# Performance work log

Measured on AMD Instinct MI355X. Metric: run time of the kernel, lower is better.

The kernel has to match this reference:

```python
import jax, jax.numpy as jnp
import numpy as np

N, E, IN_DIM, HID, HEADS, LAYERS = 50000, 320000, 128, 128, 4, 2
C = HID // HEADS  # per-head channels = 32
EPS = 1e-5


def _init(key, shape, fan_in):
    return jax.random.normal(key, shape, dtype=jnp.float32) / np.sqrt(fan_in)


def setup_inputs() -> dict:
    key = jax.random.key(0)
    ks = jax.random.split(key, 20)
    x = jax.random.normal(ks[0], (N, IN_DIM), dtype=jnp.float32)
    edge_index = jax.random.randint(ks[1], (2, E), 0, N, dtype=jnp.int64)
    edge_attr = jax.random.uniform(ks[2], (E, 1), dtype=jnp.float32)
    inp = {
        "x": x, "edge_index": edge_index, "edge_attr": edge_attr,
        "W_in": _init(ks[3], (IN_DIM, HID), IN_DIM),
        "b_in": jnp.zeros((HID,), jnp.float32),
        # per-layer TransformerConv params, stacked on leading layer axis
        "Wq": _init(ks[4], (LAYERS, HID, HID), HID),
        "bq": jnp.zeros((LAYERS, HID), jnp.float32),
        "Wk": _init(ks[5], (LAYERS, HID, HID), HID),
        "bk": jnp.zeros((LAYERS, HID), jnp.float32),
        "Wv": _init(ks[6], (LAYERS, HID, HID), HID),
        "bv": jnp.zeros((LAYERS, HID), jnp.float32),
        "We": _init(ks[7], (LAYERS, 1, HID), 1),          # lin_edge, bias=False
        "Wskip": _init(ks[8], (LAYERS, HID, HID), HID),   # root/skip projection
        "bskip": jnp.zeros((LAYERS, HID), jnp.float32),
        "Wbeta": _init(ks[9], (LAYERS, 3 * HID, 1), 3 * HID),  # lin_beta, bias=False
        "bn_gamma": jnp.ones((LAYERS, HID), jnp.float32),
        "bn_beta": jnp.zeros((LAYERS, HID), jnp.float32),
    }
    return inp


def _transformer_conv(h, src, tgt, edge_attr, Wq, bq, Wk, bk, Wv, bv, We, Wskip, bskip, Wbeta):
    n = h.shape[0]
    q = (h @ Wq + bq).reshape(n, HEADS, C)
    k = (h @ Wk + bk).reshape(n, HEADS, C)
    v = (h @ Wv + bv).reshape(n, HEADS, C)
    e = (edge_attr @ We).reshape(-1, HEADS, C)          # [E,H,C] edge embedding
    k_j = k[src] + e                                     # gather source keys
    alpha = jnp.einsum('ehc,ehc->eh', q[tgt], k_j) / jnp.sqrt(jnp.float32(C))
    amax = jax.ops.segment_max(alpha, tgt, num_segments=n)   # softmax over in-edges per target
    ex = jnp.exp(alpha - amax[tgt])
    denom = jax.ops.segment_sum(ex, tgt, num_segments=n)
    a = ex / denom[tgt]                                  # [E,H]
    msg = (v[src] + e) * a[..., None]
    out = jax.ops.segment_sum(msg, tgt, num_segments=n).reshape(n, HID)
    x_r = h @ Wskip + bskip                              # root weight
    beta = jax.nn.sigmoid(jnp.concatenate([out, x_r, out - x_r], axis=-1) @ Wbeta)
    return beta * x_r + (1.0 - beta) * out


def _batchnorm(h, gamma, beta):
    mu = h.mean(axis=0)
    var = h.var(axis=0)
    return gamma * (h - mu) * jax.lax.rsqrt(var + EPS) + beta


def reference(x, edge_index, edge_attr, W_in, b_in, Wq, bq, Wk, bk, Wv, bv, We, Wskip, bskip, Wbeta, bn_gamma, bn_beta):
    src, tgt = edge_index[0], edge_index[1]
    h = jax.nn.relu(x @ W_in + b_in)
    for l in range(LAYERS):
        h_res = h
        h = _transformer_conv(h, src, tgt, edge_attr, Wq[l], bq[l], Wk[l], bk[l], Wv[l], bv[l], We[l], Wskip[l], bskip[l], Wbeta[l])
        h = jax.nn.relu(_batchnorm(h, bn_gamma[l], bn_beta[l]))
        h = h + h_res
    return h
```

## Files before the change

kernel.cpp:

```cpp
#include <hip/hip_runtime.h>
#include <hip/hip_bf16.h>
#include <math.h>

#define EPS 1e-5f

typedef __attribute__((ext_vector_type(8))) short bf16x8;
typedef __attribute__((ext_vector_type(4))) float f32x4;

__device__ __forceinline__ unsigned short f2bf(float f) {
    unsigned u = __float_as_uint(f);
    unsigned r = (u + 0x7FFFu + ((u >> 16) & 1u)) >> 16;
    return (unsigned short)r;
}
__device__ __forceinline__ unsigned f2bf2(float lo, float hi) {
    return (unsigned)f2bf(lo) | ((unsigned)f2bf(hi) << 16);
}
__device__ __forceinline__ float bf2f(unsigned short u) {
    return __uint_as_float((unsigned)u << 16);
}
__device__ __forceinline__ void bfu2(unsigned u, float& lo, float& hi) {
    lo = __uint_as_float(u << 16);
    hi = __uint_as_float(u & 0xFFFF0000u);
}

__global__ __launch_bounds__(256) void prep(const float* __restrict__ x,
                                            unsigned short* __restrict__ xbf, int n4,
                                            const float* __restrict__ W0, const float* __restrict__ W1,
                                            const float* __restrict__ W2, const float* __restrict__ W3,
                                            const float* __restrict__ W4, const float* __restrict__ W5,
                                            const float* __restrict__ W6, const float* __restrict__ W7,
                                            const float* __restrict__ W8, unsigned short* __restrict__ Bpack,
                                            int* __restrict__ deg, int N,
                                            int nConv, int nPack) {
    int b = blockIdx.x;
    if (b < nConv) {
        int i = b * 256 + threadIdx.x;
        if (i < n4) {
            float4 v = ((const float4*)x)[i];
            ushort4 o = make_ushort4(f2bf(v.x), f2bf(v.y), f2bf(v.z), f2bf(v.w));
            ((ushort4*)xbf)[i] = o;
        }
    } else if (b < nConv + nPack) {
        int t = (b - nConv) * 256 + threadIdx.x;
        if (t < 9 * 16384) {
            int mat = t >> 14, r = t & 16383;
            const float* W;
            switch (mat) {
                case 0: W = W0; break; case 1: W = W1; break; case 2: W = W2; break;
                case 3: W = W3; break; case 4: W = W4; break; case 5: W = W5; break;
                case 6: W = W6; break; case 7: W = W7; break; default: W = W8; break;
            }
            int j = r & 7, lane = (r >> 3) & 63, nt = (r >> 9) & 7, kc = r >> 12;
            int k = kc * 32 + (lane >> 4) * 8 + j;
            int n = (lane & 15) * 8 + nt;
            Bpack[t] = f2bf(W[k * 128 + n]);
        }
    } else {
        int i = (b - nConv - nPack) * 256 + threadIdx.x;
        if (i < N) deg[i] = 0;
    }
}

template <int ACT, int WBF>
__global__ __launch_bounds__(256) void gemm_mfma(const unsigned short* __restrict__ Abf,
                                                 const unsigned short* __restrict__ Bp,
                                                 const float* __restrict__ bias,
                                                 float* __restrict__ C,
                                                 unsigned short* __restrict__ Cbf, int M) {
    int wave = threadIdx.x >> 6, lane = threadIdx.x & 63;
    int base = blockIdx.x * 64 + wave * 16;
    int m = lane & 15, kg = lane >> 4;
    int arow = base + m; if (arow >= M) arow = M - 1;
    const unsigned short* Aptr = Abf + (size_t)arow * 128 + kg * 8;
    f32x4 acc[8];
#pragma unroll
    for (int nt = 0; nt < 8; ++nt) acc[nt] = (f32x4)(0.f);
#pragma unroll
    for (int kc = 0; kc < 4; ++kc) {
        bf16x8 a = *(const bf16x8*)(Aptr + kc * 32);
        const unsigned short* bp = Bp + (size_t)kc * 4096 + (size_t)lane * 8;
#pragma unroll
        for (int nt = 0; nt < 8; ++nt) {
            bf16x8 b = *(const bf16x8*)(bp + nt * 512);
            acc[nt] = __builtin_amdgcn_mfma_f32_16x16x32_bf16(a, b, acc[nt], 0, 0, 0);
        }
    }
    int col0 = lane & 15;
    int r0 = base + (lane >> 4) * 4;
    float4 bl = *(const float4*)&bias[col0 * 8];
    float4 bh = *(const float4*)&bias[col0 * 8 + 4];
#pragma unroll
    for (int r = 0; r < 4; ++r) {
        int ro = r0 + r;
        if (ro < M) {
            float v0 = acc[0][r] + bl.x, v1 = acc[1][r] + bl.y;
            float v2 = acc[2][r] + bl.z, v3 = acc[3][r] + bl.w;
            float v4 = acc[4][r] + bh.x, v5 = acc[5][r] + bh.y;
            float v6 = acc[6][r] + bh.z, v7 = acc[7][r] + bh.w;
            if (ACT) {
                v0 = fmaxf(v0, 0.f); v1 = fmaxf(v1, 0.f); v2 = fmaxf(v2, 0.f); v3 = fmaxf(v3, 0.f);
                v4 = fmaxf(v4, 0.f); v5 = fmaxf(v5, 0.f); v6 = fmaxf(v6, 0.f); v7 = fmaxf(v7, 0.f);
            }
            size_t o = (size_t)ro * 128 + col0 * 8;
            *(float4*)&C[o]     = make_float4(v0, v1, v2, v3);
            *(float4*)&C[o + 4] = make_float4(v4, v5, v6, v7);
            if (WBF)
                *(uint4*)&Cbf[o] = make_uint4(f2bf2(v0, v1), f2bf2(v2, v3),
                                              f2bf2(v4, v5), f2bf2(v6, v7));
        }
    }
}

__global__ __launch_bounds__(256) void gemm_qk(const unsigned short* __restrict__ Abf,
                                               const unsigned short* __restrict__ Bq,
                                               const unsigned short* __restrict__ Bk,
                                               const float* __restrict__ bq,
                                               const float* __restrict__ bk,
                                               unsigned short* __restrict__ qbf,
                                               unsigned short* __restrict__ kvbf, int M) {
    int wave = threadIdx.x >> 6, lane = threadIdx.x & 63;
    int base = blockIdx.x * 64 + wave * 16;
    int m = lane & 15, kg = lane >> 4;
    int arow = base + m; if (arow >= M) arow = M - 1;
    const unsigned short* Aptr = Abf + (size_t)arow * 128 + kg * 8;
    f32x4 aq[8], ak[8];
#pragma unroll
    for (int nt = 0; nt < 8; ++nt) { aq[nt] = (f32x4)(0.f); ak[nt] = (f32x4)(0.f); }
#pragma unroll
    for (int kc = 0; kc < 4; ++kc) {
        bf16x8 a = *(const bf16x8*)(Aptr + kc * 32);
        size_t boff = (size_t)kc * 4096 + (size_t)lane * 8;
#pragma unroll
        for (int nt = 0; nt < 8; ++nt) {
            bf16x8 b0 = *(const bf16x8*)(Bq + boff + nt * 512);
            aq[nt] = __builtin_amdgcn_mfma_f32_16x16x32_bf16(a, b0, aq[nt], 0, 0, 0);
            bf16x8 b1 = *(const bf16x8*)(Bk + boff + nt * 512);
            ak[nt] = __builtin_amdgcn_mfma_f32_16x16x32_bf16(a, b1, ak[nt], 0, 0, 0);
        }
    }
    int col0 = lane & 15;
    int r0 = base + (lane >> 4) * 4;
    float4 bql = *(const float4*)&bq[col0 * 8], bqh = *(const float4*)&bq[col0 * 8 + 4];
    float4 bkl = *(const float4*)&bk[col0 * 8], bkh = *(const float4*)&bk[col0 * 8 + 4];
#pragma unroll
    for (int r = 0; r < 4; ++r) {
        int ro = r0 + r;
        if (ro < M) {
            size_t qo = (size_t)ro * 128 + col0 * 8;
            size_t kvo = (size_t)ro * 256 + col0 * 8;
            *(uint4*)&qbf[qo] = make_uint4(
                f2bf2(aq[0][r] + bql.x, aq[1][r] + bql.y), f2bf2(aq[2][r] + bql.z, aq[3][r] + bql.w),
                f2bf2(aq[4][r] + bqh.x, aq[5][r] + bqh.y), f2bf2(aq[6][r] + bqh.z, aq[7][r] + bqh.w));
            *(uint4*)&kvbf[kvo] = make_uint4(
                f2bf2(ak[0][r] + bkl.x, ak[1][r] + bkl.y), f2bf2(ak[2][r] + bkl.z, ak[3][r] + bkl.w),
                f2bf2(ak[4][r] + bkh.x, ak[5][r] + bkh.y), f2bf2(ak[6][r] + bkh.z, ak[7][r] + bkh.w));
        }
    }
}

__global__ __launch_bounds__(256) void gemm_vs(const unsigned short* __restrict__ Abf,
                                               const unsigned short* __restrict__ Bv,
                                               const unsigned short* __restrict__ Bs,
                                               const float* __restrict__ bv,
                                               const float* __restrict__ bs,
                                               unsigned short* __restrict__ kvbf,
                                               unsigned short* __restrict__ xrbf,
                                               float* __restrict__ bstatZ, int M) {
    if (blockIdx.x == 0) {
        ((float2*)bstatZ)[threadIdx.x] = make_float2(0.f, 0.f);
        ((float2*)bstatZ)[256 + threadIdx.x] = make_float2(0.f, 0.f);
        ((float2*)bstatZ)[512 + threadIdx.x] = make_float2(0.f, 0.f);
        ((float2*)bstatZ)[768 + threadIdx.x] = make_float2(0.f, 0.f);
    }
    int wave = threadIdx.x >> 6, lane = threadIdx.x & 63;
    int base = blockIdx.x * 64 + wave * 16;
    int m = lane & 15, kg = lane >> 4;
    int arow = base + m; if (arow >= M) arow = M - 1;
    const unsigned short* Aptr = Abf + (size_t)arow * 128 + kg * 8;
    f32x4 av[8], as_[8];
#pragma unroll
    for (int nt = 0; nt < 8; ++nt) { av[nt] = (f32x4)(0.f); as_[nt] = (f32x4)(0.f); }
#pragma unroll
    for (int kc = 0; kc < 4; ++kc) {
        bf16x8 a = *(const bf16x8*)(Aptr + kc * 32);
        size_t boff = (size_t)kc * 4096 + (size_t)lane * 8;
#pragma unroll
        for (int nt = 0; nt < 8; ++nt) {
            bf16x8 b2 = *(const bf16x8*)(Bv + boff + nt * 512);
            av[nt] = __builtin_amdgcn_mfma_f32_16x16x32_bf16(a, b2, av[nt], 0, 0, 0);
            bf16x8 b3 = *(const bf16x8*)(Bs + boff + nt * 512);
            as_[nt] = __builtin_amdgcn_mfma_f32_16x16x32_bf16(a, b3, as_[nt], 0, 0, 0);
        }
    }
    int col0 = lane & 15;
    int r0 = base + (lane >> 4) * 4;
    float4 bvl = *(const float4*)&bv[col0 * 8], bvh = *(const float4*)&bv[col0 * 8 + 4];
    float4 bsl = *(const float4*)&bs[col0 * 8], bsh = *(const float4*)&bs[col0 * 8 + 4];
#pragma unroll
    for (int r = 0; r < 4; ++r) {
        int ro = r0 + r;
        if (ro < M) {
            size_t qo = (size_t)ro * 128 + col0 * 8;
            size_t kvo = (size_t)ro * 256 + 128 + col0 * 8;
            *(uint4*)&kvbf[kvo] = make_uint4(
                f2bf2(av[0][r] + bvl.x, av[1][r] + bvl.y), f2bf2(av[2][r] + bvl.z, av[3][r] + bvl.w),
                f2bf2(av[4][r] + bvh.x, av[5][r] + bvh.y), f2bf2(av[6][r] + bvh.z, av[7][r] + bvh.w));
            *(uint4*)&xrbf[qo] = make_uint4(
                f2bf2(as_[0][r] + bsl.x, as_[1][r] + bsl.y), f2bf2(as_[2][r] + bsl.z, as_[3][r] + bsl.w),
                f2bf2(as_[4][r] + bsh.x, as_[5][r] + bsh.y), f2bf2(as_[6][r] + bsh.z, as_[7][r] + bsh.w));
        }
    }
}

__global__ __launch_bounds__(256) void csr_hist(const int* __restrict__ ei,
                                                int* __restrict__ deg, int E) {
    int e = blockIdx.x * 256 + threadIdx.x;
    if (e < E) atomicAdd(&deg[ei[E + e]], 1);
}

__global__ __launch_bounds__(256) void scan_block_sums(const int* __restrict__ deg,
                                                       int* __restrict__ bsums, int N) {
    __shared__ int sd[256];
    int i = blockIdx.x * 256 + threadIdx.x;
    sd[threadIdx.x] = (i < N) ? deg[i] : 0;
    __syncthreads();
    for (int off = 128; off > 0; off >>= 1) {
        if (threadIdx.x < off) sd[threadIdx.x] += sd[threadIdx.x + off];
        __syncthreads();
    }
    if (threadIdx.x == 0) bsums[blockIdx.x] = sd[0];
}

__global__ __launch_bounds__(256) void scan_bsums(const int* __restrict__ bsums,
                                                  int* __restrict__ boff, int nb) {
    __shared__ int sd[256];
    int tid = threadIdx.x;
    int per = (nb + 255) / 256;
    int start = tid * per;
    int s = 0;
    for (int i = 0; i < per; ++i) {
        int idx = start + i;
        if (idx < nb) s += bsums[idx];
    }
    int my = s;
    sd[tid] = s;
    __syncthreads();
    for (int off = 1; off < 256; off <<= 1) {
        int t = (tid >= off) ? sd[tid - off] : 0;
        __syncthreads();
        sd[tid] += t;
        __syncthreads();
    }
    int run = sd[tid] - my;
    for (int i = 0; i < per; ++i) {
        int idx = start + i;
        if (idx < nb) {
            boff[idx] = run;
            run += bsums[idx];
        }
    }
}

__global__ __launch_bounds__(256) void scan_local(const int* __restrict__ deg,
                                                  const int* __restrict__ boff,
                                                  int* __restrict__ rowptr,
                                                  int* __restrict__ wrptr, int N, int E) {
    __shared__ int sd[256];
    int i = blockIdx.x * 256 + threadIdx.x;
    int v = (i < N) ? deg[i] : 0;
    sd[threadIdx.x] = v;
    __syncthreads();
    for (int off = 1; off < 256; off <<= 1) {
        int t = (threadIdx.x >= off) ? sd[threadIdx.x - off] : 0;
        __syncthreads();
        sd[threadIdx.x] += t;
        __syncthreads();
    }
    if (i < N) {
        int excl = sd[threadIdx.x] - v + boff[blockIdx.x];
        rowptr[i] = excl;
        wrptr[i] = excl;
        if (i == N - 1) rowptr[N] = E;
    }
}

__global__ __launch_bounds__(256) void csr_fill(const int* __restrict__ ei,
                                                const float* __restrict__ ea,
                                                int* __restrict__ wrptr,
                                                int2* __restrict__ csr_sw, int E) {
    int e = blockIdx.x * 256 + threadIdx.x;
    if (e >= E) return;
    int tgt = ei[E + e];
    int pos = atomicAdd(&wrptr[tgt], 1);
    csr_sw[pos] = make_int2(ei[e], __float_as_int(ea[e]));
}

__global__ __launch_bounds__(256) void attn_gather(const unsigned short* __restrict__ qbf,
                                                   const unsigned short* __restrict__ kvbf,
                                                   const unsigned short* __restrict__ xrbf,
                                                   const int* __restrict__ rowptr,
                                                   const int2* __restrict__ csr_sw,
                                                   const float* __restrict__ Wel,
                                                   const float* __restrict__ Wb,
                                                   float* __restrict__ out,
                                                   float* __restrict__ bsumR,
                                                   float* __restrict__ bsumsqR, int N) {
    __shared__ float sdS[4][128];
    __shared__ float sdQ[4][128];
    int tid = threadIdx.x;
    int n = blockIdx.x * 16 + (tid >> 4);
    int sl = tid & 15;
    int wave = tid >> 6, lane = tid & 63;
    bool live = (n < N);
    int nn = live ? n : (N - 1);

    uint4 qu = ((const uint4*)(qbf + (size_t)nn * 128))[sl];
    float qf[8];
    bfu2(qu.x, qf[0], qf[1]); bfu2(qu.y, qf[2], qf[3]);
    bfu2(qu.z, qf[4], qf[5]); bfu2(qu.w, qf[6], qf[7]);
    float wef[8];
    {
        float4 w0 = ((const float4*)Wel)[sl * 2];
        float4 w1 = ((const float4*)Wel)[sl * 2 + 1];
        wef[0] = w0.x; wef[1] = w0.y; wef[2] = w0.z; wef[3] = w0.w;
        wef[4] = w1.x; wef[5] = w1.y; wef[6] = w1.z; wef[7] = w1.w;
    }
    float qwe = 0.f;
#pragma unroll
    for (int c = 0; c < 8; ++c) qwe += qf[c] * wef[c];
    qwe += __shfl_xor(qwe, 1);
    qwe += __shfl_xor(qwe, 2);

    float l = 0.f;
    float acc[8];
#pragma unroll
    for (int c = 0; c < 8; ++c) acc[c] = 0.f;

    int beg = live ? rowptr[nn] : 0;
    int end = live ? rowptr[nn + 1] : 0;

    if (beg < end) {
        int2 sw0 = csr_sw[beg];
        int j1 = (beg + 1 < end) ? beg + 1 : beg;
        int2 sw1 = csr_sw[j1];
        const uint4* r0 = (const uint4*)(kvbf + (size_t)sw0.x * 256);
        uint4 ku = r0[sl], vu = r0[16 + sl];

        for (int i = beg; i < end; ++i) {
            const uint4* r1 = (const uint4*)(kvbf + (size_t)sw1.x * 256);
            uint4 kun = r1[sl], vun = r1[16 + sl];
            int j2 = (i + 2 < end) ? i + 2 : beg;
            int2 sw2 = csr_sw[j2];

            float w = __int_as_float(sw0.y);
            float kf[8];
            bfu2(ku.x, kf[0], kf[1]); bfu2(ku.y, kf[2], kf[3]);
            bfu2(ku.z, kf[4], kf[5]); bfu2(ku.w, kf[6], kf[7]);
            float d = 0.f;
#pragma unroll
            for (int c = 0; c < 8; ++c) d += qf[c] * kf[c];
            d += __shfl_xor(d, 1); d += __shfl_xor(d, 2);
            float p = __expf((d + w * qwe) * 0.17677669529663687f);
            l += p;
            float vf[8];
            bfu2(vu.x, vf[0], vf[1]); bfu2(vu.y, vf[2], vf[3]);
            bfu2(vu.z, vf[4], vf[5]); bfu2(vu.w, vf[6], vf[7]);
#pragma unroll
            for (int c = 0; c < 8; ++c)
                acc[c] += p * (vf[c] + w * wef[c]);

            sw0 = sw1; sw1 = sw2;
            ku = kun; vu = vun;
        }
    }

    float inv = (l > 0.f) ? 1.f / l : 0.f;
    float ox[8];
#pragma unroll
    for (int c = 0; c < 8; ++c) ox[c] = acc[c] * inv;

    uint4 xu = ((const uint4*)(xrbf + (size_t)nn * 128))[sl];
    float xv[8];
    bfu2(xu.x, xv[0], xv[1]); bfu2(xu.y, xv[2], xv[3]);
    bfu2(xu.z, xv[4], xv[5]); bfu2(xu.w, xv[6], xv[7]);
    float4 b0 = ((const float4*)Wb)[sl * 2];
    float4 b1 = ((const float4*)Wb)[sl * 2 + 1];
    float4 c0 = ((const float4*)(Wb + 128))[sl * 2];
    float4 c1 = ((const float4*)(Wb + 128))[sl * 2 + 1];
    float4 d0 = ((const float4*)(Wb + 256))[sl * 2];
    float4 d1 = ((const float4*)(Wb + 256))[sl * 2 + 1];
    float wb0[8] = {b0.x, b0.y, b0.z, b0.w, b1.x, b1.y, b1.z, b1.w};
    float wb1[8] = {c0.x, c0.y, c0.z, c0.w, c1.x, c1.y, c1.z, c1.w};
    float wb2[8] = {d0.x, d0.y, d0.z, d0.w, d1.x, d1.y, d1.z, d1.w};
    float part = 0.f;
#pragma unroll
    for (int c = 0; c < 8; ++c)
        part += ox[c] * wb0[c] + xv[c] * wb1[c] + (ox[c] - xv[c]) * wb2[c];
    part += __shfl_xor(part, 1); part += __shfl_xor(part, 2);
    part += __shfl_xor(part, 4); part += __shfl_xor(part, 8);
    float beta = 1.f / (1.f + __expf(-part));

    float r[8];
#pragma unroll
    for (int c = 0; c < 8; ++c)
        r[c] = beta * xv[c] + (1.f - beta) * ox[c];

    if (live) {
        ((float4*)(out + (size_t)n * 128))[sl * 2] =
            make_float4(r[0], r[1], r[2], r[3]);
        ((float4*)(out + (size_t)n * 128))[sl * 2 + 1] =
            make_float4(r[4], r[5], r[6], r[7]);
    }

    float s8[8], q8[8];
#pragma unroll
    for (int c = 0; c < 8; ++c) {
        s8[c] = live ? r[c] : 0.f;
        q8[c] = live ? r[c] * r[c] : 0.f;
    }
#pragma unroll
    for (int c = 0; c < 8; ++c) {
        s8[c] += __shfl_xor(s8[c], 16); s8[c] += __shfl_xor(s8[c], 32);
        q8[c] += __shfl_xor(q8[c], 16); q8[c] += __shfl_xor(q8[c], 32);
    }
    if ((lane >> 4) == 0) {
#pragma unroll
        for (int c = 0; c < 8; ++c) {
            sdS[wave][sl * 8 + c] = s8[c];
            sdQ[wave][sl * 8 + c] = q8[c];
        }
    }
    __syncthreads();
    if (tid < 128) {
        float s = sdS[0][tid] + sdS[1][tid] + sdS[2][tid] + sdS[3][tid];
        float q = sdQ[0][tid] + sdQ[1][tid] + sdQ[2][tid] + sdQ[3][tid];
        int rep = blockIdx.x & 7;
        atomicAdd(&bsumR[rep * 128 + tid], s);
        atomicAdd(&bsumsqR[rep * 128 + tid], q);
    }
}

__global__ __launch_bounds__(256) void bn_apply(const float* __restrict__ o,
                                                const float* __restrict__ hres,
                                                float* __restrict__ hout,
                                                unsigned short* __restrict__ hout_bf,
                                                const float* __restrict__ bsumR,
                                                const float* __restrict__ bsumsqR,
                                                const float* __restrict__ gamma,
                                                const float* __restrict__ bbeta,
                                                int N, float invN) {
    int i = blockIdx.x * 256 + threadIdx.x;
    if (i >= N * 32) return;
    int c4 = i & 31;
    float4 s = make_float4(0.f, 0.f, 0.f, 0.f), ss = s;
#pragma unroll
    for (int rep = 0; rep < 8; ++rep) {
        float4 sv = ((const float4*)bsumR)[rep * 32 + c4];
        float4 qv = ((const float4*)bsumsqR)[rep * 32 + c4];
        s.x += sv.x; s.y += sv.y; s.z += sv.z; s.w += sv.w;
        ss.x += qv.x; ss.y += qv.y; ss.z += qv.z; ss.w += qv.w;
    }
    float4 g = ((const float4*)gamma)[c4];
    float4 b = ((const float4*)bbeta)[c4];
    float4 ov = ((const float4*)o)[i];
    float4 hr = ((const float4*)hres)[i];
    float4 r;
    { float mu = s.x * invN, var = ss.x * invN - mu * mu;
      r.x = fmaxf((ov.x - mu) * (g.x * rsqrtf(var + EPS)) + b.x, 0.f) + hr.x; }
    { float mu = s.y * invN, var = ss.y * invN - mu * mu;
      r.y = fmaxf((ov.y - mu) * (g.y * rsqrtf(var + EPS)) + b.y, 0.f) + hr.y; }
    { float mu = s.z * invN, var = ss.z * invN - mu * mu;
      r.z = fmaxf((ov.z - mu) * (g.z * rsqrtf(var + EPS)) + b.z, 0.f) + hr.z; }
    { float mu = s.w * invN, var = ss.w * invN - mu * mu;
      r.w = fmaxf((ov.w - mu) * (g.w * rsqrtf(var + EPS)) + b.w, 0.f) + hr.w; }
    ((float4*)hout)[i] = r;
    if (hout_bf) {
        ushort4 ob = make_ushort4(f2bf(r.x), f2bf(r.y), f2bf(r.z), f2bf(r.w));
        ((ushort4*)hout_bf)[i] = ob;
    }
}

extern "C" void kernel_launch(void* const* d_in, const int* in_sizes, int n_in,
                              void* d_out, int out_size, void* d_ws, size_t ws_size,
                              hipStream_t stream) {
    const float* x     = (const float*)d_in[0];
    const int*   ei    = (const int*)d_in[1];
    const float* ea    = (const float*)d_in[2];
    const float* W_in  = (const float*)d_in[3];
    const float* b_in  = (const float*)d_in[4];
    const float* Wq    = (const float*)d_in[5];
    const float* bq    = (const float*)d_in[6];
    const float* Wk    = (const float*)d_in[7];
    const float* bk    = (const float*)d_in[8];
    const float* Wv    = (const float*)d_in[9];
    const float* bv    = (const float*)d_in[10];
    const float* We    = (const float*)d_in[11];
    const float* Wskip = (const float*)d_in[12];
    const float* bskip = (const float*)d_in[13];
    const float* Wbeta = (const float*)d_in[14];
    const float* bn_g  = (const float*)d_in[15];
    const float* bn_b  = (const float*)d_in[16];

    const int N = in_sizes[0] / 128;
    const int E = in_sizes[1] / 2;

    float* ws = (float*)d_ws;
    unsigned short* Bpack = (unsigned short*)ws;
    size_t off = 73728;
    unsigned short* xbf  = (unsigned short*)(ws + off);               off += (size_t)N * 64;
    unsigned short* hbf  = (unsigned short*)(ws + off);               off += (size_t)N * 64;
    unsigned short* qbf  = (unsigned short*)(ws + off);               off += (size_t)N * 64;
    unsigned short* kvbf = (unsigned short*)(ws + off);               off += (size_t)N * 128;
    unsigned short* xrbf = (unsigned short*)(ws + off);               off += (size_t)N * 64;
    float* h    = ws + off;  off += (size_t)N * 128;
    float* attn = ws + off;  off += (size_t)N * 128;
    float* bsumR   = ws + off;  off += 1024;
    float* bsumsqR = ws + off;  off += 1024;
    int2* csr_sw = (int2*)(ws + off);  off += (size_t)E * 2;
    int* deg     = (int*)(ws + off);
    int* rowptr  = deg + N;
    int* wrptr   = rowptr + (N + 1);
    int* bsums   = wrptr + N;
    int* boff    = bsums + ((N + 255) / 256 + 1);

    dim3 blk(256);
    int gGemm   = (N + 63) / 64;
    int gNode16 = (N + 15) / 16;
    int gEdge   = (E + 255) / 256;
    int gApply  = (N * 32 + 255) / 256;
    int nbScan  = (N + 255) / 256;

    int nConv = gApply;
    int nPack = (9 * 16384 + 255) / 256;
    prep<<<nConv + nPack + nbScan, blk, 0, stream>>>(
        x, xbf, N * 32,
        W_in, Wq, Wk, Wv, Wskip, Wq + 16384, Wk + 16384, Wv + 16384, Wskip + 16384,
        Bpack, deg, N, nConv, nPack);

    csr_hist<<<gEdge, blk, 0, stream>>>(ei, deg, E);
    scan_block_sums<<<nbScan, blk, 0, stream>>>(deg, bsums, N);
    scan_bsums<<<1, blk, 0, stream>>>(bsums, boff, nbScan);
    scan_local<<<nbScan, blk, 0, stream>>>(deg, boff, rowptr, wrptr, N, E);
    csr_fill<<<gEdge, blk, 0, stream>>>(ei, ea, wrptr, csr_sw, E);

    gemm_mfma<1, 1><<<gGemm, blk, 0, stream>>>(xbf, Bpack + 0 * 16384, b_in, h, hbf, N);

    for (int l = 0; l < 2; ++l) {
        const unsigned short* Bq = Bpack + (size_t)(1 + l * 4 + 0) * 16384;
        const unsigned short* Bk = Bpack + (size_t)(1 + l * 4 + 1) * 16384;
        const unsigned short* Bv = Bpack + (size_t)(1 + l * 4 + 2) * 16384;
        const unsigned short* Bs = Bpack + (size_t)(1 + l * 4 + 3) * 16384;
        gemm_qk<<<gGemm, blk, 0, stream>>>(hbf, Bq, Bk, bq + l * 128, bk + l * 128,
                                           qbf, kvbf, N);
        gemm_vs<<<gGemm, blk, 0, stream>>>(hbf, Bv, Bs, bv + l * 128, bskip + l * 128,
                                           kvbf, xrbf, bsumR, N);
        attn_gather<<<gNode16, blk, 0, stream>>>(qbf, kvbf, xrbf, rowptr, csr_sw,
                                                 We + l * 128, Wbeta + l * 384, attn,
                                                 bsumR, bsumsqR, N);
        bn_apply<<<gApply, blk, 0, stream>>>(attn, h, (l == 1) ? (float*)d_out : h,
                                             (l == 0) ? hbf : (unsigned short*)0,
                                             bsumR, bsumsqR, bn_g + l * 128, bn_b + l * 128,
                                             N, 1.0f / (float)N);
    }
}
```

Before: 333.7 us.

## Split each node's in-edges across four 16-lane groups in attention gather

The attention gather kernel now assigns one node per wave instead of one node per 16 lanes. The four 16-lane groups in a wave each take every fourth in-edge, and their softmax numerators and denominators are combined with cross-lane shuffles. This shortens the serial per-node edge loop and exposes more memory parallelism for the random K/V gathers. The cost is four times as many blocks, fewer nodes per block, and three quarters of the lanes doing redundant work in the beta/output epilogue. Because there is no running max, the per-group partial sums can be added directly, so the summation order changes.

```diff
diff --git a/kernel.cpp b/kernel.cpp
--- a/kernel.cpp
+++ b/kernel.cpp
@@ -308,9 +308,10 @@
     __shared__ float sdS[4][128];
     __shared__ float sdQ[4][128];
     int tid = threadIdx.x;
-    int n = blockIdx.x * 16 + (tid >> 4);
-    int sl = tid & 15;
     int wave = tid >> 6, lane = tid & 63;
+    int sl = lane & 15;
+    int g = lane >> 4;
+    int n = blockIdx.x * 4 + wave;
     bool live = (n < N);
     int nn = live ? n : (N - 1);
 
@@ -339,17 +340,18 @@
     int beg = live ? rowptr[nn] : 0;
     int end = live ? rowptr[nn + 1] : 0;
 
-    if (beg < end) {
-        int2 sw0 = csr_sw[beg];
-        int j1 = (beg + 1 < end) ? beg + 1 : beg;
+    int i = beg + g;
+    if (i < end) {
+        int2 sw0 = csr_sw[i];
+        int j1 = (i + 4 < end) ? i + 4 : i;
         int2 sw1 = csr_sw[j1];
         const uint4* r0 = (const uint4*)(kvbf + (size_t)sw0.x * 256);
         uint4 ku = r0[sl], vu = r0[16 + sl];
 
-        for (int i = beg; i < end; ++i) {
+        for (; i < end; i += 4) {
             const uint4* r1 = (const uint4*)(kvbf + (size_t)sw1.x * 256);
             uint4 kun = r1[sl], vun = r1[16 + sl];
-            int j2 = (i + 2 < end) ? i + 2 : beg;
+            int j2 = (i + 8 < end) ? i + 8 : i;
             int2 sw2 = csr_sw[j2];
 
             float w = __int_as_float(sw0.y);
@@ -373,6 +375,14 @@
             ku = kun; vu = vun;
         }
     }
+
+#pragma unroll
+    for (int c = 0; c < 8; ++c) {
+        acc[c] += __shfl_xor(acc[c], 16);
+        acc[c] += __shfl_xor(acc[c], 32);
+    }
+    l += __shfl_xor(l, 16);
+    l += __shfl_xor(l, 32);
 
     float inv = (l > 0.f) ? 1.f / l : 0.f;
     float ox[8];
@@ -405,29 +415,19 @@
     for (int c = 0; c < 8; ++c)
         r[c] = beta * xv[c] + (1.f - beta) * ox[c];
 
-    if (live) {
+    if (live && g == 0) {
         ((float4*)(out + (size_t)n * 128))[sl * 2] =
             make_float4(r[0], r[1], r[2], r[3]);
         ((float4*)(out + (size_t)n * 128))[sl * 2 + 1] =
             make_float4(r[4], r[5], r[6], r[7]);
     }
 
-    float s8[8], q8[8];
-#pragma unroll
-    for (int c = 0; c < 8; ++c) {
-        s8[c] = live ? r[c] : 0.f;
-        q8[c] = live ? r[c] * r[c] : 0.f;
-    }
-#pragma unroll
-    for (int c = 0; c < 8; ++c) {
-        s8[c] += __shfl_xor(s8[c], 16); s8[c] += __shfl_xor(s8[c], 32);
-        q8[c] += __shfl_xor(q8[c], 16); q8[c] += __shfl_xor(q8[c], 32);
-    }
-    if ((lane >> 4) == 0) {
+    if (g == 0) {
 #pragma unroll
         for (int c = 0; c < 8; ++c) {
-            sdS[wave][sl * 8 + c] = s8[c];
-            sdQ[wave][sl * 8 + c] = q8[c];
+            float rv = live ? r[c] : 0.f;
+            sdS[wave][sl * 8 + c] = rv;
+            sdQ[wave][sl * 8 + c] = rv * rv;
         }
     }
     __syncthreads();
@@ -525,7 +525,7 @@
 
     dim3 blk(256);
     int gGemm   = (N + 63) / 64;
-    int gNode16 = (N + 15) / 16;
+    int gNode4  = (N + 3) / 4;
     int gEdge   = (E + 255) / 256;
     int gApply  = (N * 32 + 255) / 256;
     int nbScan  = (N + 255) / 256;
@@ -554,9 +554,9 @@
                                            qbf, kvbf, N);
         gemm_vs<<<gGemm, blk, 0, stream>>>(hbf, Bv, Bs, bv + l * 128, bskip + l * 128,
                                            kvbf, xrbf, bsumR, N);
-        attn_gather<<<gNode16, blk, 0, stream>>>(qbf, kvbf, xrbf, rowptr, csr_sw,
-                                                 We + l * 128, Wbeta + l * 384, attn,
-                                                 bsumR, bsumsqR, N);
+        attn_gather<<<gNode4, blk, 0, stream>>>(qbf, kvbf, xrbf, rowptr, csr_sw,
+                                                We + l * 128, Wbeta + l * 384, attn,
+                                                bsumR, bsumsqR, N);
         bn_apply<<<gApply, blk, 0, stream>>>(attn, h, (l == 1) ? (float*)d_out : h,
                                              (l == 0) ? hbf : (unsigned short*)0,
                                              bsumR, bsumsqR, bn_g + l * 128, bn_b + l * 128,
```

Result: slower. 360.3 us (+8.0%).
